# Performance work log

Hardware: AMD Instinct MI355X
Metric: run time of the kernel (lower is better)

## Reference

```python
import jax, jax.numpy as jnp
import numpy as np

NY, NX = 320, 320
NT = 160
SHOTS, NSRC, NREC = 2, 8, 96
DT = 4.0e-4
DH = 4.0
PML_W = 20
MAX_VEL = 1600.0
C1, C2 = 9.0 / 8.0, -1.0 / 24.0  # 4th-order staggered-grid FD coefficients


def _profile(n, w, d0):
    d = np.zeros(n, np.float64)
    i = np.arange(n, dtype=np.float64)
    d[:w] = d0 * ((w - i[:w]) / w) ** 2
    d[n - w:] = d0 * ((i[n - w:] - (n - 1 - w)) / w) ** 2
    return d


def _pml_b():
    # PML damping profile d(x) = d0*(x/L)^2, CPML decay factor b = exp(-d*dt)
    d0 = 3.0 * MAX_VEL * np.log(1000.0) / (2.0 * PML_W * DH)
    by = np.exp(-_profile(NY, PML_W, d0) * DT).astype(np.float32)
    bx = np.exp(-_profile(NX, PML_W, d0) * DT).astype(np.float32)
    return jnp.asarray(by)[None, :, None], jnp.asarray(bx)[None, None, :]


def _edge_mask():
    # mirrors zero_edges: kill wraparound contamination at the grid border
    m = np.ones((NY, NX), np.float32)
    m[:2, :] = 0.0
    m[-2:, :] = 0.0
    m[:, :2] = 0.0
    m[:, -2:] = 0.0
    return jnp.asarray(m)


def _d(f, axis, fwd):
    # staggered 4th-order forward (D+) / backward (D-) difference along axis
    if fwd:
        return (C1 * (jnp.roll(f, -1, axis) - f)
                + C2 * (jnp.roll(f, -2, axis) - jnp.roll(f, 1, axis))) * (1.0 / DH)
    return (C1 * (f - jnp.roll(f, 1, axis))
            + C2 * (jnp.roll(f, -1, axis) - jnp.roll(f, 2, axis))) * (1.0 / DH)


def _simulate(lamb, mu, buoyancy, amps, src_loc, rec_loc, checkpoint=False):
    by, bx = _pml_b()
    mask = _edge_mask()
    lam2mu = lamb + 2.0 * mu
    bidx = jnp.arange(SHOTS)[:, None]
    sy, sx = src_loc[..., 0], src_loc[..., 1]
    ry, rx = rec_loc[..., 0], rec_loc[..., 1]
    src_buoy = buoyancy[sy, sx]  # [shot, nsrc]
    zero = jnp.zeros((SHOTS, NY, NX), lamb.dtype)
    carry0 = tuple(zero for _ in range(13))

    def step(c, amp_t):
        (vy, vx, syy, sxy, sxx,
         mvyy, mvyx, mvxy, mvxx,
         msyyy, msxyy, msxyx, msxxx) = c
        # --- velocity update (with CPML memory variables) ---
        d = _d(syy, 1, False)
        msyyy = by * msyyy + (by - 1.0) * d
        ay = d + msyyy
        d = _d(sxy, 2, True)
        msxyx = bx * msxyx + (bx - 1.0) * d
        ay = ay + d + msxyx
        vy = vy + DT * buoyancy * ay
        d = _d(sxx, 2, False)
        msxxx = bx * msxxx + (bx - 1.0) * d
        ax = d + msxxx
        d = _d(sxy, 1, True)
        msxyy = by * msxyy + (by - 1.0) * d
        ax = ax + d + msxyy
        vx = vx + DT * buoyancy * ax
        # --- inject y-oriented sources into vy ---
        vy = vy.at[bidx, sy, sx].add(DT * amp_t * src_buoy)
        vy = vy * mask
        vx = vx * mask
        # --- stress update ---
        d = _d(vy, 1, True)
        mvyy = by * mvyy + (by - 1.0) * d
        e1 = d + mvyy
        d = _d(vx, 2, False)
        mvxx = bx * mvxx + (bx - 1.0) * d
        e2 = d + mvxx
        syy = (syy + DT * (lam2mu * e1 + lamb * e2)) * mask
        sxx = (sxx + DT * (lam2mu * e2 + lamb * e1)) * mask
        d = _d(vy, 2, True)
        mvyx = bx * mvyx + (bx - 1.0) * d
        g = d + mvyx
        d = _d(vx, 1, False)
        mvxy = by * mvxy + (by - 1.0) * d
        g = g + d + mvxy
        sxy = (sxy + DT * mu * g) * mask
        rec = vy[bidx, ry, rx]  # [shot, nrec]
        return (vy, vx, syy, sxy, sxx, mvyy, mvyx, mvxy, mvxx,
                msyyy, msxyy, msxyx, msxxx), rec

    f = jax.checkpoint(step) if checkpoint else step
    _, recs = jax.lax.scan(f, carry0, jnp.transpose(amps, (2, 0, 1)))
    # velocity receivers sampled at t+/-1/2 -> average adjacent time samples
    recs = (recs[1:] + recs[:-1]) * 0.5  # [nt-1, shot, nrec]
    return jnp.transpose(recs, (1, 2, 0))  # [shot, nrec, nt-1]


def setup_inputs() -> dict:
    key = jax.random.key(0)
    k1, k2, k3, k4, k5, k6 = jax.random.split(key, 6)
    u_l = jax.random.uniform(k1, (NY, NX), jnp.float32)
    u_m = jax.random.uniform(k2, (NY, NX), jnp.float32)
    u_b = jax.random.uniform(k3, (NY, NX), jnp.float32)
    lamb = (2.0e9 * (1.0 + 0.2 * u_l)).astype(jnp.float32)
    mu = (0.8e9 * (1.0 + 0.2 * u_m)).astype(jnp.float32)
    buoyancy = (1.0 / (1800.0 + 400.0 * u_b)).astype(jnp.float32)
    source_amplitudes_y = jax.random.normal(k4, (SHOTS, NSRC, NT), jnp.float32)
    source_locations_y = jax.random.randint(k5, (SHOTS, NSRC, 2), PML_W + 4, NY - PML_W - 4)
    receiver_locations_y = jax.random.randint(k6, (SHOTS, NREC, 2), PML_W + 4, NY - PML_W - 4)
    return {
        'lamb': lamb, 'mu': mu, 'buoyancy': buoyancy,
        'source_amplitudes_y': source_amplitudes_y,
        'source_locations_y': source_locations_y,
        'receiver_locations_y': receiver_locations_y,
    }


def reference(lamb, mu, buoyancy, source_amplitudes_y,
              source_locations_y, receiver_locations_y):
    return _simulate(lamb, mu, buoyancy, source_amplitudes_y,
                     source_locations_y, receiver_locations_y)
```

## Files before the change

kernel.cpp:

```cpp
#include <hip/hip_runtime.h>
#include <math.h>

constexpr int NY_ = 320, NX_ = 320, NT_ = 160, SHOTS_ = 2, NSRC_ = 8, NREC_ = 96;
constexpr float DT_  = 4.0e-4f;
constexpr float C1_  = 9.0f / 8.0f;
constexpr float C2_  = -1.0f / 24.0f;
constexpr float IDH_ = 0.25f;
constexpr int NP_     = NY_ * NX_;
constexpr int NSTRIP_ = 40;
constexpr int NBLK_   = SHOTS_ * NSTRIP_;
constexpr int REC_OFF_ = 8 * NP_;
constexpr int FLG_OFF_ = 8 * NP_ + SHOTS_ * NREC_ * NT_;
constexpr int WS_WORDS_ = FLG_OFF_ + 256;

__device__ __forceinline__ float cld(const float* p) {
    return __hip_atomic_load(p, __ATOMIC_RELAXED, __HIP_MEMORY_SCOPE_AGENT);
}
__device__ __forceinline__ void cst(float* p, float v) {
    __hip_atomic_store(p, v, __ATOMIC_RELAXED, __HIP_MEMORY_SCOPE_AGENT);
}
__device__ __forceinline__ unsigned cldu(const unsigned* p) {
    return __hip_atomic_load(p, __ATOMIC_RELAXED, __HIP_MEMORY_SCOPE_AGENT);
}
__device__ __forceinline__ void cstu(unsigned* p, unsigned v) {
    __hip_atomic_store(p, v, __ATOMIC_RELAXED, __HIP_MEMORY_SCOPE_AGENT);
}

__device__ __forceinline__ float gldf(const float* p, int y, int c) {
    return ((unsigned)y < (unsigned)NY_) ? cld(p + y * NX_ + c) : 0.0f;
}
__device__ __forceinline__ float ltap(const float (*A)[NX_], int ly, int c) {
    return ((unsigned)c < (unsigned)NX_) ? A[ly][c] : 0.0f;
}
__device__ __forceinline__ float shtap(float cur, float adj, int lane, int dx) {
    int idx = (lane + dx) & 63;
    float a = __shfl(cur, idx, 64);
    float b = __shfl(adj, idx, 64);
    return ((unsigned)(lane + dx) < 64u) ? a : b;
}

__device__ __forceinline__ void pollNbr(const unsigned* f, int sbase, int j,
                                        unsigned tgt, int tid) {
    __syncthreads();
    if (tid < 64) {
        for (;;) {
            bool ok = true;
            if (tid == 0 && j > 0)           ok = cldu(&f[sbase + j - 1]) >= tgt;
            else if (tid == 1 && j < NSTRIP_ - 1) ok = cldu(&f[sbase + j + 1]) >= tgt;
            if (__all(ok)) break;
            __builtin_amdgcn_s_sleep(1);
        }
    }
    __syncthreads();
    asm volatile("" ::: "memory");
}

__global__ void init_kernel(float* __restrict__ ws) {
    for (int i = blockIdx.x * 256 + threadIdx.x; i < WS_WORDS_; i += gridDim.x * 256)
        ws[i] = 0.0f;
}

__global__ __launch_bounds__(512)
void elastic_kernel(const float* __restrict__ lamb, const float* __restrict__ mu,
                    const float* __restrict__ buoy, const float* __restrict__ amps,
                    const int* __restrict__ src_loc, const int* __restrict__ rec_loc,
                    float* __restrict__ out, float* __restrict__ ws)
{
    __shared__ float Lvy[12][NX_], Lvx[12][NX_], Lsyy[12][NX_], Lsxy[12][NX_];

    const int tid  = threadIdx.x;
    const int lane = tid & 63;
    const int w    = tid >> 6;
    const int bid  = blockIdx.x;
    const int s    = bid / NSTRIP_;
    const int j    = bid % NSTRIP_;
    const int r0   = j * 8;
    const int gy   = r0 + w;
    const int ly   = w + 2;

    float* gVy  = ws + (0 * SHOTS_ + s) * NP_;
    float* gVx  = ws + (1 * SHOTS_ + s) * NP_;
    float* gSyy = ws + (2 * SHOTS_ + s) * NP_;
    float* gSxy = ws + (3 * SHOTS_ + s) * NP_;
    float* recp = ws + REC_OFF_ + (s * NREC_ + tid) * NT_;
    unsigned* flgV = (unsigned*)(ws + FLG_OFF_);
    unsigned* flgS = flgV + NBLK_;
    const int sbase = s * NSTRIP_;

    const double d0 = 3.0 * 1600.0 * log(1000.0) / (2.0 * 20.0 * 4.0);
    double py = 0.0;
    if (gy < 20)             { double u = (20.0 - gy) / 20.0;           py = u * u; }
    else if (gy >= NY_ - 20) { double u = (gy - (NY_ - 1 - 20)) / 20.0; py = u * u; }
    const float by = (float)exp(-d0 * py * 4.0e-4);
    const float bym1 = by - 1.0f;

    float bx[5], bxm1[5], mk[5], la[5], muv[5], bu[5], l2m[5];
    #pragma unroll
    for (int k = 0; k < 5; ++k) {
        int c = 64 * k + lane;
        double px = 0.0;
        if (c < 20)             { double u = (20.0 - c) / 20.0;           px = u * u; }
        else if (c >= NX_ - 20) { double u = (c - (NX_ - 1 - 20)) / 20.0; px = u * u; }
        bx[k] = (float)exp(-d0 * px * 4.0e-4);
        bxm1[k] = bx[k] - 1.0f;
        mk[k] = (gy < 2 || gy >= NY_ - 2 || c < 2 || c >= NX_ - 2) ? 0.0f : 1.0f;
        la[k]  = lamb[gy * NX_ + c];
        muv[k] = mu[gy * NX_ + c];
        bu[k]  = buoy[gy * NX_ + c];
        l2m[k] = la[k] + 2.0f * muv[k];
    }

    unsigned long long sm = 0ull;
    for (int js = 0; js < NSRC_; ++js) {
        int sy = src_loc[(s * NSRC_ + js) * 2 + 0];
        int sx = src_loc[(s * NSRC_ + js) * 2 + 1];
        if (sy == gy && (sx & 63) == lane) sm |= 1ull << (8 * (sx >> 6) + js);
    }
    bool myrec = false; int rl = 0;
    if (tid < NREC_) {
        int ry = rec_loc[(s * NREC_ + tid) * 2 + 0];
        int rx = rec_loc[(s * NREC_ + tid) * 2 + 1];
        if ((ry >> 3) == j) { myrec = true; rl = ((ry & 7) + 2) * NX_ + rx; }
    }

    for (int i = tid; i < 12 * NX_; i += 512) {
        ((float*)Lvy)[i] = 0.f; ((float*)Lvx)[i] = 0.f;
        ((float*)Lsyy)[i] = 0.f; ((float*)Lsxy)[i] = 0.f;
    }

    float vy[5] = {}, vx[5] = {}, syy[5] = {}, sxy[5] = {}, sxx[5] = {};
    float msyyy[5] = {}, msxyy[5] = {}, msxyx[5] = {}, msxxx[5] = {};
    float mvyy[5] = {}, mvyx[5] = {}, mvxy[5] = {}, mvxx[5] = {};

    for (int t = 0; t < NT_; ++t) {
        pollNbr(flgS, sbase, j, (unsigned)t, tid);

        if (tid < NX_) {
            int c = tid;
            float a0 = gldf(gSyy, r0 - 2, c), a1 = gldf(gSyy, r0 - 1, c), a2 = gldf(gSyy, r0 + 8, c);
            float b0 = gldf(gSxy, r0 - 1, c), b1 = gldf(gSxy, r0 + 8, c), b2 = gldf(gSxy, r0 + 9, c);
            Lsyy[0][c] = a0; Lsyy[1][c] = a1; Lsyy[10][c] = a2;
            Lsxy[1][c] = b0; Lsxy[10][c] = b1; Lsxy[11][c] = b2;
        }
        __syncthreads();

        #pragma unroll
        for (int k = 0; k < 5; ++k) {
            const int c = 64 * k + lane;
            const float sxxp = (k < 4) ? sxx[k + 1] : 0.0f;
            const float sxxm = (k > 0) ? sxx[k - 1] : 0.0f;
            float d, ay, ax;
            d = (C1_ * (syy[k] - Lsyy[ly - 1][c]) + C2_ * (Lsyy[ly + 1][c] - Lsyy[ly - 2][c])) * IDH_;
            msyyy[k] = by * msyyy[k] + bym1 * d;
            ay = d + msyyy[k];
            d = (C1_ * (ltap(Lsxy, ly, c + 1) - sxy[k])
               + C2_ * (ltap(Lsxy, ly, c + 2) - ltap(Lsxy, ly, c - 1))) * IDH_;
            msxyx[k] = bx[k] * msxyx[k] + bxm1[k] * d;
            ay = ay + d + msxyx[k];
            vy[k] = vy[k] + DT_ * bu[k] * ay;
            d = (C1_ * (sxx[k] - shtap(sxx[k], sxxm, lane, -1))
               + C2_ * (shtap(sxx[k], sxxp, lane, 1) - shtap(sxx[k], sxxm, lane, -2))) * IDH_;
            msxxx[k] = bx[k] * msxxx[k] + bxm1[k] * d;
            ax = d + msxxx[k];
            d = (C1_ * (Lsxy[ly + 1][c] - sxy[k]) + C2_ * (Lsxy[ly + 2][c] - Lsxy[ly - 1][c])) * IDH_;
            msxyy[k] = by * msxyy[k] + bym1 * d;
            ax = ax + d + msxyy[k];
            vx[k] = vx[k] + DT_ * bu[k] * ax;
            unsigned m = (unsigned)(sm >> (8 * k)) & 0xFFu;
            if (m) {
                for (int js = 0; js < NSRC_; ++js)
                    if (m & (1u << js)) vy[k] += DT_ * amps[(s * NSRC_ + js) * NT_ + t] * bu[k];
            }
            vy[k] *= mk[k]; vx[k] *= mk[k];
            Lvy[ly][c] = vy[k]; Lvx[ly][c] = vx[k];
        }
        __syncthreads();

        if (myrec) recp[t] = ((const float*)Lvy)[rl];

        if (tid < NX_) {
            int c = tid;
            float v0 = Lvy[2][c], v1 = Lvy[3][c], v2 = Lvy[9][c];
            float u0 = Lvx[2][c], u1 = Lvx[8][c], u2 = Lvx[9][c];
            cst(&gVy[(r0 + 0) * NX_ + c], v0);
            cst(&gVy[(r0 + 1) * NX_ + c], v1);
            cst(&gVy[(r0 + 7) * NX_ + c], v2);
            cst(&gVx[(r0 + 0) * NX_ + c], u0);
            cst(&gVx[(r0 + 6) * NX_ + c], u1);
            cst(&gVx[(r0 + 7) * NX_ + c], u2);
        }
        __syncthreads();
        if (tid == 0) {
            asm volatile("s_waitcnt vmcnt(0)" ::: "memory");
            cstu(&flgV[sbase + j], (unsigned)(t + 1));
        }

        pollNbr(flgV, sbase, j, (unsigned)(t + 1), tid);

        if (tid < NX_) {
            int c = tid;
            float a0 = gldf(gVy, r0 - 1, c), a1 = gldf(gVy, r0 + 8, c), a2 = gldf(gVy, r0 + 9, c);
            float b0 = gldf(gVx, r0 - 2, c), b1 = gldf(gVx, r0 - 1, c), b2 = gldf(gVx, r0 + 8, c);
            Lvy[1][c] = a0; Lvy[10][c] = a1; Lvy[11][c] = a2;
            Lvx[0][c] = b0; Lvx[1][c] = b1; Lvx[10][c] = b2;
        }
        __syncthreads();

        #pragma unroll
        for (int k = 0; k < 5; ++k) {
            const int c = 64 * k + lane;
            float d, e1, e2, g;
            d = (C1_ * (Lvy[ly + 1][c] - vy[k]) + C2_ * (Lvy[ly + 2][c] - Lvy[ly - 1][c])) * IDH_;
            mvyy[k] = by * mvyy[k] + bym1 * d;
            e1 = d + mvyy[k];
            d = (C1_ * (vx[k] - ltap(Lvx, ly, c - 1))
               + C2_ * (ltap(Lvx, ly, c + 1) - ltap(Lvx, ly, c - 2))) * IDH_;
            mvxx[k] = bx[k] * mvxx[k] + bxm1[k] * d;
            e2 = d + mvxx[k];
            syy[k] = (syy[k] + DT_ * (l2m[k] * e1 + la[k] * e2)) * mk[k];
            sxx[k] = (sxx[k] + DT_ * (l2m[k] * e2 + la[k] * e1)) * mk[k];
            d = (C1_ * (ltap(Lvy, ly, c + 1) - vy[k])
               + C2_ * (ltap(Lvy, ly, c + 2) - ltap(Lvy, ly, c - 1))) * IDH_;
            mvyx[k] = bx[k] * mvyx[k] + bxm1[k] * d;
            g = d + mvyx[k];
            d = (C1_ * (vx[k] - Lvx[ly - 1][c]) + C2_ * (Lvx[ly + 1][c] - Lvx[ly - 2][c])) * IDH_;
            mvxy[k] = by * mvxy[k] + bym1 * d;
            g = g + d + mvxy[k];
            sxy[k] = (sxy[k] + DT_ * muv[k] * g) * mk[k];
            Lsyy[ly][c] = syy[k]; Lsxy[ly][c] = sxy[k];
        }
        __syncthreads();

        if (tid < NX_) {
            int c = tid;
            float a0 = Lsyy[2][c], a1 = Lsyy[8][c], a2 = Lsyy[9][c];
            float b0 = Lsxy[2][c], b1 = Lsxy[3][c], b2 = Lsxy[9][c];
            cst(&gSyy[(r0 + 0) * NX_ + c], a0);
            cst(&gSyy[(r0 + 6) * NX_ + c], a1);
            cst(&gSyy[(r0 + 7) * NX_ + c], a2);
            cst(&gSxy[(r0 + 0) * NX_ + c], b0);
            cst(&gSxy[(r0 + 1) * NX_ + c], b1);
            cst(&gSxy[(r0 + 7) * NX_ + c], b2);
        }
        __syncthreads();
        if (tid == 0) {
            asm volatile("s_waitcnt vmcnt(0)" ::: "memory");
            cstu(&flgS[sbase + j], (unsigned)(t + 1));
        }
    }

    if (myrec) {
        float* op = out + (s * NREC_ + tid) * (NT_ - 1);
        for (int t = 0; t < NT_ - 1; ++t) op[t] = 0.5f * (recp[t] + recp[t + 1]);
    }
}

extern "C" void kernel_launch(void* const* d_in, const int* in_sizes, int n_in,
                              void* d_out, int out_size, void* d_ws, size_t ws_size,
                              hipStream_t stream)
{
    const float* lamb = (const float*)d_in[0];
    const float* mu   = (const float*)d_in[1];
    const float* buoy = (const float*)d_in[2];
    const float* amps = (const float*)d_in[3];
    const int*   src  = (const int*)d_in[4];
    const int*   recl = (const int*)d_in[5];
    float* out = (float*)d_out;
    float* ws  = (float*)d_ws;

    init_kernel<<<dim3(512), dim3(256), 0, stream>>>(ws);
    elastic_kernel<<<dim3(NBLK_), dim3(512), 0, stream>>>(lamb, mu, buoy, amps, src, recl, out, ws);
}
```

Before: 1.321 ms.

## Halve inter-block syncs per step via redundant halo-row velocity computation

Each block now runs 12 waves (768 threads) covering its 8 rows plus 2-row halos. It recomputes the velocity rows its neighbours own, so the per-timestep exchange shrinks to one stress-halo handoff instead of separate velocity and stress handoffs. Stress halo rows, including sxx, are written to double-buffered per-strip slots in the workspace rather than to full global fields. This cuts the neighbour flag polling and global round-trips per step from two to one, at the cost of redundant halo compute, larger blocks and more register/LDS pressure.

```diff
diff --git a/kernel.cpp b/kernel.cpp
--- a/kernel.cpp
+++ b/kernel.cpp
@@ -6,12 +6,16 @@
 constexpr float C1_  = 9.0f / 8.0f;
 constexpr float C2_  = -1.0f / 24.0f;
 constexpr float IDH_ = 0.25f;
-constexpr int NP_     = NY_ * NX_;
 constexpr int NSTRIP_ = 40;
 constexpr int NBLK_   = SHOTS_ * NSTRIP_;
-constexpr int REC_OFF_ = 8 * NP_;
-constexpr int FLG_OFF_ = 8 * NP_ + SHOTS_ * NREC_ * NT_;
+constexpr int HSLOT_   = 15 * NX_;
+constexpr int REC_OFF_ = 2 * SHOTS_ * NSTRIP_ * HSLOT_;
+constexpr int FLG_OFF_ = REC_OFF_ + SHOTS_ * NREC_ * NT_;
 constexpr int WS_WORDS_ = FLG_OFF_ + 256;
+
+__device__ __forceinline__ int hoff(int p, int s, int j) {
+    return ((p * SHOTS_ + s) * NSTRIP_ + j) * HSLOT_;
+}
 
 __device__ __forceinline__ float cld(const float* p) {
     return __hip_atomic_load(p, __ATOMIC_RELAXED, __HIP_MEMORY_SCOPE_AGENT);
@@ -26,9 +30,7 @@
     __hip_atomic_store(p, v, __ATOMIC_RELAXED, __HIP_MEMORY_SCOPE_AGENT);
 }
 
-__device__ __forceinline__ float gldf(const float* p, int y, int c) {
-    return ((unsigned)y < (unsigned)NY_) ? cld(p + y * NX_ + c) : 0.0f;
-}
+template <int R>
 __device__ __forceinline__ float ltap(const float (*A)[NX_], int ly, int c) {
     return ((unsigned)c < (unsigned)NX_) ? A[ly][c] : 0.0f;
 }
@@ -45,7 +47,7 @@
     if (tid < 64) {
         for (;;) {
             bool ok = true;
-            if (tid == 0 && j > 0)           ok = cldu(&f[sbase + j - 1]) >= tgt;
+            if (tid == 0 && j > 0)                ok = cldu(&f[sbase + j - 1]) >= tgt;
             else if (tid == 1 && j < NSTRIP_ - 1) ok = cldu(&f[sbase + j + 1]) >= tgt;
             if (__all(ok)) break;
             __builtin_amdgcn_s_sleep(1);
@@ -60,13 +62,13 @@
         ws[i] = 0.0f;
 }
 
-__global__ __launch_bounds__(512)
+__global__ __launch_bounds__(768)
 void elastic_kernel(const float* __restrict__ lamb, const float* __restrict__ mu,
                     const float* __restrict__ buoy, const float* __restrict__ amps,
                     const int* __restrict__ src_loc, const int* __restrict__ rec_loc,
                     float* __restrict__ out, float* __restrict__ ws)
 {
-    __shared__ float Lvy[12][NX_], Lvx[12][NX_], Lsyy[12][NX_], Lsxy[12][NX_];
+    __shared__ float Lsyy[14][NX_], Lsxy[14][NX_], Lvy[11][NX_], Lvx[11][NX_];
 
     const int tid  = threadIdx.x;
     const int lane = tid & 63;
@@ -75,16 +77,15 @@
     const int s    = bid / NSTRIP_;
     const int j    = bid % NSTRIP_;
     const int r0   = j * 8;
-    const int gy   = r0 + w;
-    const int ly   = w + 2;
-
-    float* gVy  = ws + (0 * SHOTS_ + s) * NP_;
-    float* gVx  = ws + (1 * SHOTS_ + s) * NP_;
-    float* gSyy = ws + (2 * SHOTS_ + s) * NP_;
-    float* gSxy = ws + (3 * SHOTS_ + s) * NP_;
+    const int gy   = r0 - 2 + w;
+    const int ys   = w + 1;
+    const bool doVy = (w >= 1);
+    const bool doVx = (w <= 10);
+    const bool doS  = (w >= 2 && w <= 9);
+
+    float* H = ws;
     float* recp = ws + REC_OFF_ + (s * NREC_ + tid) * NT_;
-    unsigned* flgV = (unsigned*)(ws + FLG_OFF_);
-    unsigned* flgS = flgV + NBLK_;
+    unsigned* flg = (unsigned*)(ws + FLG_OFF_);
     const int sbase = s * NSTRIP_;
 
     const double d0 = 3.0 * 1600.0 * log(1000.0) / (2.0 * 20.0 * 4.0);
@@ -93,6 +94,7 @@
     else if (gy >= NY_ - 20) { double u = (gy - (NY_ - 1 - 20)) / 20.0; py = u * u; }
     const float by = (float)exp(-d0 * py * 4.0e-4);
     const float bym1 = by - 1.0f;
+    const int gyc = gy < 0 ? 0 : (gy > NY_ - 1 ? NY_ - 1 : gy);
 
     float bx[5], bxm1[5], mk[5], la[5], muv[5], bu[5], l2m[5];
     #pragma unroll
@@ -104,9 +106,9 @@
         bx[k] = (float)exp(-d0 * px * 4.0e-4);
         bxm1[k] = bx[k] - 1.0f;
         mk[k] = (gy < 2 || gy >= NY_ - 2 || c < 2 || c >= NX_ - 2) ? 0.0f : 1.0f;
-        la[k]  = lamb[gy * NX_ + c];
-        muv[k] = mu[gy * NX_ + c];
-        bu[k]  = buoy[gy * NX_ + c];
+        la[k]  = lamb[gyc * NX_ + c];
+        muv[k] = mu[gyc * NX_ + c];
+        bu[k]  = buoy[gyc * NX_ + c];
         l2m[k] = la[k] + 2.0f * muv[k];
     }
 
@@ -116,136 +118,141 @@
         int sx = src_loc[(s * NSRC_ + js) * 2 + 1];
         if (sy == gy && (sx & 63) == lane) sm |= 1ull << (8 * (sx >> 6) + js);
     }
-    bool myrec = false; int rl = 0;
+    bool myrec = false; int rrow = 0, rx = 0;
     if (tid < NREC_) {
         int ry = rec_loc[(s * NREC_ + tid) * 2 + 0];
-        int rx = rec_loc[(s * NREC_ + tid) * 2 + 1];
-        if ((ry >> 3) == j) { myrec = true; rl = ((ry & 7) + 2) * NX_ + rx; }
-    }
-
-    for (int i = tid; i < 12 * NX_; i += 512) {
-        ((float*)Lvy)[i] = 0.f; ((float*)Lvx)[i] = 0.f;
-        ((float*)Lsyy)[i] = 0.f; ((float*)Lsxy)[i] = 0.f;
-    }
+        rx     = rec_loc[(s * NREC_ + tid) * 2 + 1];
+        if ((ry >> 3) == j) { myrec = true; rrow = ry - r0 + 1; }
+    }
+
+    for (int i = tid; i < 14 * NX_; i += 768) { ((float*)Lsyy)[i] = 0.f; ((float*)Lsxy)[i] = 0.f; }
+    for (int i = tid; i < 11 * NX_; i += 768) { ((float*)Lvy)[i] = 0.f; ((float*)Lvx)[i] = 0.f; }
 
     float vy[5] = {}, vx[5] = {}, syy[5] = {}, sxy[5] = {}, sxx[5] = {};
     float msyyy[5] = {}, msxyy[5] = {}, msxyx[5] = {}, msxxx[5] = {};
     float mvyy[5] = {}, mvyx[5] = {}, mvxy[5] = {}, mvxx[5] = {};
 
     for (int t = 0; t < NT_; ++t) {
-        pollNbr(flgS, sbase, j, (unsigned)t, tid);
+        pollNbr(flg, sbase, j, (unsigned)t, tid);
+        const int pi = (t + 1) & 1;
+        const int po = t & 1;
 
         if (tid < NX_) {
             int c = tid;
-            float a0 = gldf(gSyy, r0 - 2, c), a1 = gldf(gSyy, r0 - 1, c), a2 = gldf(gSyy, r0 + 8, c);
-            float b0 = gldf(gSxy, r0 - 1, c), b1 = gldf(gSxy, r0 + 8, c), b2 = gldf(gSxy, r0 + 9, c);
-            Lsyy[0][c] = a0; Lsyy[1][c] = a1; Lsyy[10][c] = a2;
-            Lsxy[1][c] = b0; Lsxy[10][c] = b1; Lsxy[11][c] = b2;
+            if (j > 0) {
+                const float* b = H + hoff(pi, s, j - 1);
+                float a0 = cld(b + 3 * NX_ + c), a1 = cld(b + 4 * NX_ + c), a2 = cld(b + 5 * NX_ + c);
+                float d0_ = cld(b + 9 * NX_ + c), d1 = cld(b + 10 * NX_ + c), d2 = cld(b + 11 * NX_ + c);
+                Lsyy[0][c] = a0; Lsyy[1][c] = a1; Lsyy[2][c] = a2;
+                Lsxy[0][c] = d0_; Lsxy[1][c] = d1; Lsxy[2][c] = d2;
+            }
+            if (j < NSTRIP_ - 1) {
+                const float* b = H + hoff(pi, s, j + 1);
+                float a0 = cld(b + 0 * NX_ + c), a1 = cld(b + 1 * NX_ + c), a2 = cld(b + 2 * NX_ + c);
+                float d0_ = cld(b + 6 * NX_ + c), d1 = cld(b + 7 * NX_ + c), d2 = cld(b + 8 * NX_ + c);
+                Lsyy[11][c] = a0; Lsyy[12][c] = a1; Lsyy[13][c] = a2;
+                Lsxy[11][c] = d0_; Lsxy[12][c] = d1; Lsxy[13][c] = d2;
+            }
+        }
+        if (w == 0 && j > 0) {
+            const float* b = H + hoff(pi, s, j - 1) + 13 * NX_;
+            #pragma unroll
+            for (int k = 0; k < 5; ++k) sxx[k] = cld(b + 64 * k + lane);
+        } else if (w == 1 && j > 0) {
+            const float* b = H + hoff(pi, s, j - 1) + 14 * NX_;
+            #pragma unroll
+            for (int k = 0; k < 5; ++k) sxx[k] = cld(b + 64 * k + lane);
+        } else if (w == 10 && j < NSTRIP_ - 1) {
+            const float* b = H + hoff(pi, s, j + 1) + 12 * NX_;
+            #pragma unroll
+            for (int k = 0; k < 5; ++k) sxx[k] = cld(b + 64 * k + lane);
         }
         __syncthreads();
 
-        #pragma unroll
-        for (int k = 0; k < 5; ++k) {
-            const int c = 64 * k + lane;
-            const float sxxp = (k < 4) ? sxx[k + 1] : 0.0f;
-            const float sxxm = (k > 0) ? sxx[k - 1] : 0.0f;
-            float d, ay, ax;
-            d = (C1_ * (syy[k] - Lsyy[ly - 1][c]) + C2_ * (Lsyy[ly + 1][c] - Lsyy[ly - 2][c])) * IDH_;
-            msyyy[k] = by * msyyy[k] + bym1 * d;
-            ay = d + msyyy[k];
-            d = (C1_ * (ltap(Lsxy, ly, c + 1) - sxy[k])
-               + C2_ * (ltap(Lsxy, ly, c + 2) - ltap(Lsxy, ly, c - 1))) * IDH_;
-            msxyx[k] = bx[k] * msxyx[k] + bxm1[k] * d;
-            ay = ay + d + msxyx[k];
-            vy[k] = vy[k] + DT_ * bu[k] * ay;
-            d = (C1_ * (sxx[k] - shtap(sxx[k], sxxm, lane, -1))
-               + C2_ * (shtap(sxx[k], sxxp, lane, 1) - shtap(sxx[k], sxxm, lane, -2))) * IDH_;
-            msxxx[k] = bx[k] * msxxx[k] + bxm1[k] * d;
-            ax = d + msxxx[k];
-            d = (C1_ * (Lsxy[ly + 1][c] - sxy[k]) + C2_ * (Lsxy[ly + 2][c] - Lsxy[ly - 1][c])) * IDH_;
-            msxyy[k] = by * msxyy[k] + bym1 * d;
-            ax = ax + d + msxyy[k];
-            vx[k] = vx[k] + DT_ * bu[k] * ax;
-            unsigned m = (unsigned)(sm >> (8 * k)) & 0xFFu;
-            if (m) {
-                for (int js = 0; js < NSRC_; ++js)
-                    if (m & (1u << js)) vy[k] += DT_ * amps[(s * NSRC_ + js) * NT_ + t] * bu[k];
-            }
-            vy[k] *= mk[k]; vx[k] *= mk[k];
-            Lvy[ly][c] = vy[k]; Lvx[ly][c] = vx[k];
+        if (doVy) {
+            #pragma unroll
+            for (int k = 0; k < 5; ++k) {
+                const int c = 64 * k + lane;
+                float d, ay;
+                d = (C1_ * (Lsyy[ys][c] - Lsyy[ys - 1][c]) + C2_ * (Lsyy[ys + 1][c] - Lsyy[ys - 2][c])) * IDH_;
+                msyyy[k] = by * msyyy[k] + bym1 * d;
+                ay = d + msyyy[k];
+                d = (C1_ * (ltap<0>(Lsxy, ys, c + 1) - Lsxy[ys][c])
+                   + C2_ * (ltap<0>(Lsxy, ys, c + 2) - ltap<0>(Lsxy, ys, c - 1))) * IDH_;
+                msxyx[k] = bx[k] * msxyx[k] + bxm1[k] * d;
+                ay = ay + d + msxyx[k];
+                vy[k] = vy[k] + DT_ * bu[k] * ay;
+                unsigned m = (unsigned)(sm >> (8 * k)) & 0xFFu;
+                if (m) {
+                    for (int js = 0; js < NSRC_; ++js)
+                        if (m & (1u << js)) vy[k] += DT_ * amps[(s * NSRC_ + js) * NT_ + t] * bu[k];
+                }
+                vy[k] *= mk[k];
+                Lvy[w - 1][c] = vy[k];
+            }
+        }
+        if (doVx) {
+            #pragma unroll
+            for (int k = 0; k < 5; ++k) {
+                const int c = 64 * k + lane;
+                const float sxxp = (k < 4) ? sxx[k + 1] : 0.0f;
+                const float sxxm = (k > 0) ? sxx[k - 1] : 0.0f;
+                float d, ax;
+                d = (C1_ * (sxx[k] - shtap(sxx[k], sxxm, lane, -1))
+                   + C2_ * (shtap(sxx[k], sxxp, lane, 1) - shtap(sxx[k], sxxm, lane, -2))) * IDH_;
+                msxxx[k] = bx[k] * msxxx[k] + bxm1[k] * d;
+                ax = d + msxxx[k];
+                d = (C1_ * (Lsxy[ys + 1][c] - Lsxy[ys][c]) + C2_ * (Lsxy[ys + 2][c] - Lsxy[ys - 1][c])) * IDH_;
+                msxyy[k] = by * msxyy[k] + bym1 * d;
+                ax = ax + d + msxyy[k];
+                vx[k] = vx[k] + DT_ * bu[k] * ax;
+                vx[k] *= mk[k];
+                Lvx[w][c] = vx[k];
+            }
         }
         __syncthreads();
 
-        if (myrec) recp[t] = ((const float*)Lvy)[rl];
-
-        if (tid < NX_) {
-            int c = tid;
-            float v0 = Lvy[2][c], v1 = Lvy[3][c], v2 = Lvy[9][c];
-            float u0 = Lvx[2][c], u1 = Lvx[8][c], u2 = Lvx[9][c];
-            cst(&gVy[(r0 + 0) * NX_ + c], v0);
-            cst(&gVy[(r0 + 1) * NX_ + c], v1);
-            cst(&gVy[(r0 + 7) * NX_ + c], v2);
-            cst(&gVx[(r0 + 0) * NX_ + c], u0);
-            cst(&gVx[(r0 + 6) * NX_ + c], u1);
-            cst(&gVx[(r0 + 7) * NX_ + c], u2);
+        if (myrec) recp[t] = Lvy[rrow][rx];
+
+        if (doS) {
+            const int yv = w - 1, xv = w;
+            float* Hj = H + hoff(po, s, j);
+            const int slotS = (w <= 4) ? (w - 2) : (w - 4);
+            #pragma unroll
+            for (int k = 0; k < 5; ++k) {
+                const int c = 64 * k + lane;
+                float d, e1, e2, g;
+                d = (C1_ * (Lvy[yv + 1][c] - vy[k]) + C2_ * (Lvy[yv + 2][c] - Lvy[yv - 1][c])) * IDH_;
+                mvyy[k] = by * mvyy[k] + bym1 * d;
+                e1 = d + mvyy[k];
+                d = (C1_ * (vx[k] - ltap<0>(Lvx, xv, c - 1))
+                   + C2_ * (ltap<0>(Lvx, xv, c + 1) - ltap<0>(Lvx, xv, c - 2))) * IDH_;
+                mvxx[k] = bx[k] * mvxx[k] + bxm1[k] * d;
+                e2 = d + mvxx[k];
+                syy[k] = (syy[k] + DT_ * (l2m[k] * e1 + la[k] * e2)) * mk[k];
+                sxx[k] = (sxx[k] + DT_ * (l2m[k] * e2 + la[k] * e1)) * mk[k];
+                d = (C1_ * (ltap<0>(Lvy, yv, c + 1) - vy[k])
+                   + C2_ * (ltap<0>(Lvy, yv, c + 2) - ltap<0>(Lvy, yv, c - 1))) * IDH_;
+                mvyx[k] = bx[k] * mvyx[k] + bxm1[k] * d;
+                g = d + mvyx[k];
+                d = (C1_ * (vx[k] - Lvx[xv - 1][c]) + C2_ * (Lvx[xv + 1][c] - Lvx[xv - 2][c])) * IDH_;
+                mvxy[k] = by * mvxy[k] + bym1 * d;
+                g = g + d + mvxy[k];
+                sxy[k] = (sxy[k] + DT_ * muv[k] * g) * mk[k];
+                Lsyy[ys][c] = syy[k]; Lsxy[ys][c] = sxy[k];
+                if (w <= 4 || w >= 7) {
+                    cst(Hj + slotS * NX_ + c, syy[k]);
+                    cst(Hj + (6 + slotS) * NX_ + c, sxy[k]);
+                }
+                if (w == 2) cst(Hj + 12 * NX_ + c, sxx[k]);
+                else if (w == 8) cst(Hj + 13 * NX_ + c, sxx[k]);
+                else if (w == 9) cst(Hj + 14 * NX_ + c, sxx[k]);
+            }
         }
         __syncthreads();
         if (tid == 0) {
             asm volatile("s_waitcnt vmcnt(0)" ::: "memory");
-            cstu(&flgV[sbase + j], (unsigned)(t + 1));
-        }
-
-        pollNbr(flgV, sbase, j, (unsigned)(t + 1), tid);
-
-        if (tid < NX_) {
-            int c = tid;
-            float a0 = gldf(gVy, r0 - 1, c), a1 = gldf(gVy, r0 + 8, c), a2 = gldf(gVy, r0 + 9, c);
-            float b0 = gldf(gVx, r0 - 2, c), b1 = gldf(gVx, r0 - 1, c), b2 = gldf(gVx, r0 + 8, c);
-            Lvy[1][c] = a0; Lvy[10][c] = a1; Lvy[11][c] = a2;
-            Lvx[0][c] = b0; Lvx[1][c] = b1; Lvx[10][c] = b2;
-        }
-        __syncthreads();
-
-        #pragma unroll
-        for (int k = 0; k < 5; ++k) {
-            const int c = 64 * k + lane;
-            float d, e1, e2, g;
-            d = (C1_ * (Lvy[ly + 1][c] - vy[k]) + C2_ * (Lvy[ly + 2][c] - Lvy[ly - 1][c])) * IDH_;
-            mvyy[k] = by * mvyy[k] + bym1 * d;
-            e1 = d + mvyy[k];
-            d = (C1_ * (vx[k] - ltap(Lvx, ly, c - 1))
-               + C2_ * (ltap(Lvx, ly, c + 1) - ltap(Lvx, ly, c - 2))) * IDH_;
-            mvxx[k] = bx[k] * mvxx[k] + bxm1[k] * d;
-            e2 = d + mvxx[k];
-            syy[k] = (syy[k] + DT_ * (l2m[k] * e1 + la[k] * e2)) * mk[k];
-            sxx[k] = (sxx[k] + DT_ * (l2m[k] * e2 + la[k] * e1)) * mk[k];
-            d = (C1_ * (ltap(Lvy, ly, c + 1) - vy[k])
-               + C2_ * (ltap(Lvy, ly, c + 2) - ltap(Lvy, ly, c - 1))) * IDH_;
-            mvyx[k] = bx[k] * mvyx[k] + bxm1[k] * d;
-            g = d + mvyx[k];
-            d = (C1_ * (vx[k] - Lvx[ly - 1][c]) + C2_ * (Lvx[ly + 1][c] - Lvx[ly - 2][c])) * IDH_;
-            mvxy[k] = by * mvxy[k] + bym1 * d;
-            g = g + d + mvxy[k];
-            sxy[k] = (sxy[k] + DT_ * muv[k] * g) * mk[k];
-            Lsyy[ly][c] = syy[k]; Lsxy[ly][c] = sxy[k];
-        }
-        __syncthreads();
-
-        if (tid < NX_) {
-            int c = tid;
-            float a0 = Lsyy[2][c], a1 = Lsyy[8][c], a2 = Lsyy[9][c];
-            float b0 = Lsxy[2][c], b1 = Lsxy[3][c], b2 = Lsxy[9][c];
-            cst(&gSyy[(r0 + 0) * NX_ + c], a0);
-            cst(&gSyy[(r0 + 6) * NX_ + c], a1);
-            cst(&gSyy[(r0 + 7) * NX_ + c], a2);
-            cst(&gSxy[(r0 + 0) * NX_ + c], b0);
-            cst(&gSxy[(r0 + 1) * NX_ + c], b1);
-            cst(&gSxy[(r0 + 7) * NX_ + c], b2);
-        }
-        __syncthreads();
-        if (tid == 0) {
-            asm volatile("s_waitcnt vmcnt(0)" ::: "memory");
-            cstu(&flgS[sbase + j], (unsigned)(t + 1));
+            cstu(&flg[sbase + j], (unsigned)(t + 1));
         }
     }
 
@@ -269,5 +276,5 @@
     float* ws  = (float*)d_ws;
 
     init_kernel<<<dim3(512), dim3(256), 0, stream>>>(ws);
-    elastic_kernel<<<dim3(NBLK_), dim3(512), 0, stream>>>(lamb, mu, buoy, amps, src, recl, out, ws);
-}
+    elastic_kernel<<<dim3(NBLK_), dim3(768), 0, stream>>>(lamb, mu, buoy, amps, src, recl, out, ws);
+}
```

After: 1.935 ms. +46.5%, slower.

## Replace block barriers with per-wave LDS flags and double-buffered halo slots

Applied to the files above, without the earlier changes.

Removes all __syncthreads from the time loop. Waves now coordinate through per-wave LDS flags with acquire/release, and only the boundary waves (0,1,6,7) exchange halos with neighbouring strips. That exchange goes through compact double-buffered slot buffers with per-role global flags instead of full-grid arrays. x-direction stencil taps now use wavefront shuffles of register values instead of LDS reads, and receivers are recorded directly from registers. The goal is to cut block-wide barrier and polling latency so interior waves can run ahead, at the cost of more complex fine-grained spin-waiting and a higher risk of memory-ordering bugs.

```diff
diff --git a/kernel.cpp b/kernel.cpp
--- a/kernel.cpp
+++ b/kernel.cpp
@@ -6,12 +6,14 @@
 constexpr float C1_  = 9.0f / 8.0f;
 constexpr float C2_  = -1.0f / 24.0f;
 constexpr float IDH_ = 0.25f;
-constexpr int NP_     = NY_ * NX_;
 constexpr int NSTRIP_ = 40;
 constexpr int NBLK_   = SHOTS_ * NSTRIP_;
-constexpr int REC_OFF_ = 8 * NP_;
-constexpr int FLG_OFF_ = 8 * NP_ + SHOTS_ * NREC_ * NT_;
-constexpr int WS_WORDS_ = FLG_OFF_ + 256;
+constexpr int SLOT_    = 6 * NX_;
+constexpr int VS_OFF_  = 0;
+constexpr int SS_OFF_  = VS_OFF_ + 2 * SHOTS_ * NSTRIP_ * SLOT_;
+constexpr int REC_OFF_ = SS_OFF_ + 2 * SHOTS_ * NSTRIP_ * SLOT_;
+constexpr int GF_OFF_  = REC_OFF_ + SHOTS_ * NREC_ * NT_;
+constexpr int WS_WORDS_ = GF_OFF_ + 8 * NBLK_ + 64;
 
 __device__ __forceinline__ float cld(const float* p) {
     return __hip_atomic_load(p, __ATOMIC_RELAXED, __HIP_MEMORY_SCOPE_AGENT);
@@ -25,12 +27,15 @@
 __device__ __forceinline__ void cstu(unsigned* p, unsigned v) {
     __hip_atomic_store(p, v, __ATOMIC_RELAXED, __HIP_MEMORY_SCOPE_AGENT);
 }
-
-__device__ __forceinline__ float gldf(const float* p, int y, int c) {
-    return ((unsigned)y < (unsigned)NY_) ? cld(p + y * NX_ + c) : 0.0f;
-}
-__device__ __forceinline__ float ltap(const float (*A)[NX_], int ly, int c) {
-    return ((unsigned)c < (unsigned)NX_) ? A[ly][c] : 0.0f;
+__device__ __forceinline__ void lwait(const unsigned* f, unsigned tgt) {
+    while (__hip_atomic_load(f, __ATOMIC_ACQUIRE, __HIP_MEMORY_SCOPE_WORKGROUP) < tgt) {}
+}
+__device__ __forceinline__ void lpost(unsigned* f, unsigned v) {
+    __hip_atomic_store(f, v, __ATOMIC_RELEASE, __HIP_MEMORY_SCOPE_WORKGROUP);
+}
+__device__ __forceinline__ void gwait2(const unsigned* a, const unsigned* b, unsigned tgt) {
+    while (cldu(a) < tgt || cldu(b) < tgt) __builtin_amdgcn_s_sleep(1);
+    asm volatile("" ::: "memory");
 }
 __device__ __forceinline__ float shtap(float cur, float adj, int lane, int dx) {
     int idx = (lane + dx) & 63;
@@ -39,53 +44,26 @@
     return ((unsigned)(lane + dx) < 64u) ? a : b;
 }
 
-__device__ __forceinline__ void pollNbr(const unsigned* f, int sbase, int j,
-                                        unsigned tgt, int tid) {
-    __syncthreads();
-    if (tid < 64) {
-        for (;;) {
-            bool ok = true;
-            if (tid == 0 && j > 0)           ok = cldu(&f[sbase + j - 1]) >= tgt;
-            else if (tid == 1 && j < NSTRIP_ - 1) ok = cldu(&f[sbase + j + 1]) >= tgt;
-            if (__all(ok)) break;
-            __builtin_amdgcn_s_sleep(1);
-        }
-    }
-    __syncthreads();
-    asm volatile("" ::: "memory");
-}
-
 __global__ void init_kernel(float* __restrict__ ws) {
     for (int i = blockIdx.x * 256 + threadIdx.x; i < WS_WORDS_; i += gridDim.x * 256)
         ws[i] = 0.0f;
 }
 
-__global__ __launch_bounds__(512)
+__global__ __launch_bounds__(512, 2)
 void elastic_kernel(const float* __restrict__ lamb, const float* __restrict__ mu,
                     const float* __restrict__ buoy, const float* __restrict__ amps,
                     const int* __restrict__ src_loc, const int* __restrict__ rec_loc,
                     float* __restrict__ out, float* __restrict__ ws)
 {
-    __shared__ float Lvy[12][NX_], Lvx[12][NX_], Lsyy[12][NX_], Lsxy[12][NX_];
-
-    const int tid  = threadIdx.x;
-    const int lane = tid & 63;
-    const int w    = tid >> 6;
-    const int bid  = blockIdx.x;
-    const int s    = bid / NSTRIP_;
-    const int j    = bid % NSTRIP_;
-    const int r0   = j * 8;
-    const int gy   = r0 + w;
-    const int ly   = w + 2;
-
-    float* gVy  = ws + (0 * SHOTS_ + s) * NP_;
-    float* gVx  = ws + (1 * SHOTS_ + s) * NP_;
-    float* gSyy = ws + (2 * SHOTS_ + s) * NP_;
-    float* gSxy = ws + (3 * SHOTS_ + s) * NP_;
-    float* recp = ws + REC_OFF_ + (s * NREC_ + tid) * NT_;
-    unsigned* flgV = (unsigned*)(ws + FLG_OFF_);
-    unsigned* flgS = flgV + NBLK_;
-    const int sbase = s * NSTRIP_;
+    __shared__ float Lsyy[12][NX_], Lsxy[12][NX_], Lvy[12][NX_], Lvx[12][NX_];
+    __shared__ unsigned vF[8], sF[8], hF[4];
+
+    const int tid = threadIdx.x, lane = tid & 63, w = tid >> 6;
+    const int bid = blockIdx.x, s = bid / NSTRIP_, j = bid % NSTRIP_;
+    const int r0 = j * 8, gy = r0 + w, yi = w + 2;
+    const int sj = s * NSTRIP_ + j;
+    unsigned* gV = (unsigned*)(ws + GF_OFF_);
+    unsigned* gS = gV + 4 * NBLK_;
 
     const double d0 = 3.0 * 1600.0 * log(1000.0) / (2.0 * 20.0 * 4.0);
     double py = 0.0;
@@ -109,60 +87,91 @@
         bu[k]  = buoy[gy * NX_ + c];
         l2m[k] = la[k] + 2.0f * muv[k];
     }
-
     unsigned long long sm = 0ull;
     for (int js = 0; js < NSRC_; ++js) {
         int sy = src_loc[(s * NSRC_ + js) * 2 + 0];
         int sx = src_loc[(s * NSRC_ + js) * 2 + 1];
         if (sy == gy && (sx & 63) == lane) sm |= 1ull << (8 * (sx >> 6) + js);
     }
-    bool myrec = false; int rl = 0;
-    if (tid < NREC_) {
-        int ry = rec_loc[(s * NREC_ + tid) * 2 + 0];
-        int rx = rec_loc[(s * NREC_ + tid) * 2 + 1];
-        if ((ry >> 3) == j) { myrec = true; rl = ((ry & 7) + 2) * NX_ + rx; }
-    }
+    int nrec = 0, recid[8], reck[8];
+    for (int r = 0; r < NREC_; ++r) {
+        int ry = rec_loc[(s * NREC_ + r) * 2 + 0];
+        int rx = rec_loc[(s * NREC_ + r) * 2 + 1];
+        if (ry == gy && (rx & 63) == lane && nrec < 8) { recid[nrec] = r; reck[nrec] = rx >> 6; ++nrec; }
+    }
+    float* recbase = ws + REC_OFF_;
 
     for (int i = tid; i < 12 * NX_; i += 512) {
-        ((float*)Lvy)[i] = 0.f; ((float*)Lvx)[i] = 0.f;
         ((float*)Lsyy)[i] = 0.f; ((float*)Lsxy)[i] = 0.f;
-    }
+        ((float*)Lvy)[i]  = 0.f; ((float*)Lvx)[i]  = 0.f;
+    }
+    if (tid < 8) { vF[tid] = 0u; sF[tid] = 0u; }
+    if (tid < 4) hF[tid] = 0u;
+    __syncthreads();
 
     float vy[5] = {}, vx[5] = {}, syy[5] = {}, sxy[5] = {}, sxx[5] = {};
     float msyyy[5] = {}, msxyy[5] = {}, msxyx[5] = {}, msxxx[5] = {};
     float mvyy[5] = {}, mvyx[5] = {}, mvxy[5] = {}, mvxx[5] = {};
 
     for (int t = 0; t < NT_; ++t) {
-        pollNbr(flgS, sbase, j, (unsigned)t, tid);
-
-        if (tid < NX_) {
-            int c = tid;
-            float a0 = gldf(gSyy, r0 - 2, c), a1 = gldf(gSyy, r0 - 1, c), a2 = gldf(gSyy, r0 + 8, c);
-            float b0 = gldf(gSxy, r0 - 1, c), b1 = gldf(gSxy, r0 + 8, c), b2 = gldf(gSxy, r0 + 9, c);
-            Lsyy[0][c] = a0; Lsyy[1][c] = a1; Lsyy[10][c] = a2;
-            Lsxy[1][c] = b0; Lsxy[10][c] = b1; Lsxy[11][c] = b2;
-        }
-        __syncthreads();
+        const unsigned ut = (unsigned)t;
+        const int pi = (t + 1) & 1, po = t & 1;
+
+        if (w == 0) {
+            if (j > 0) {
+                lwait(&vF[1], ut);
+                gwait2(&gS[2 * NBLK_ + (sj - 1)], &gS[3 * NBLK_ + (sj - 1)], ut);
+                const float* B = ws + SS_OFF_ + ((pi * SHOTS_ + s) * NSTRIP_ + (j - 1)) * SLOT_;
+                #pragma unroll
+                for (int k = 0; k < 5; ++k) {
+                    int c = 64 * k + lane;
+                    float a = cld(B + 3 * NX_ + c), b = cld(B + 4 * NX_ + c), e = cld(B + 5 * NX_ + c);
+                    Lsyy[0][c] = a; Lsyy[1][c] = b; Lsxy[1][c] = e;
+                }
+            }
+            lpost(&hF[0], ut + 1u);
+        } else if (w == 7) {
+            if (j < NSTRIP_ - 1) {
+                lwait(&vF[6], ut);
+                gwait2(&gS[0 * NBLK_ + (sj + 1)], &gS[1 * NBLK_ + (sj + 1)], ut);
+                const float* B = ws + SS_OFF_ + ((pi * SHOTS_ + s) * NSTRIP_ + (j + 1)) * SLOT_;
+                #pragma unroll
+                for (int k = 0; k < 5; ++k) {
+                    int c = 64 * k + lane;
+                    float a = cld(B + 0 * NX_ + c), b = cld(B + 1 * NX_ + c), e = cld(B + 2 * NX_ + c);
+                    Lsyy[10][c] = a; Lsxy[10][c] = b; Lsxy[11][c] = e;
+                }
+            }
+            lpost(&hF[1], ut + 1u);
+        }
+        if (w == 1) lwait(&hF[0], ut + 1u);
+        if (w == 6) lwait(&hF[1], ut + 1u);
+        if (w >= 2) lwait(&sF[w - 2], ut);
+        if (w >= 1) lwait(&sF[w - 1], ut);
+        if (w <= 6) lwait(&sF[w + 1], ut);
+        if (w <= 5) lwait(&sF[w + 2], ut);
 
         #pragma unroll
         for (int k = 0; k < 5; ++k) {
             const int c = 64 * k + lane;
-            const float sxxp = (k < 4) ? sxx[k + 1] : 0.0f;
-            const float sxxm = (k > 0) ? sxx[k - 1] : 0.0f;
+            const float sxyP = (k < 4) ? sxy[k + 1] : 0.0f;
+            const float sxyM = (k > 0) ? sxy[k - 1] : 0.0f;
+            const float sxxP = (k < 4) ? sxx[k + 1] : 0.0f;
+            const float sxxM = (k > 0) ? sxx[k - 1] : 0.0f;
             float d, ay, ax;
-            d = (C1_ * (syy[k] - Lsyy[ly - 1][c]) + C2_ * (Lsyy[ly + 1][c] - Lsyy[ly - 2][c])) * IDH_;
+            d = (C1_ * (syy[k] - Lsyy[yi - 1][c]) + C2_ * (Lsyy[yi + 1][c] - Lsyy[yi - 2][c])) * IDH_;
             msyyy[k] = by * msyyy[k] + bym1 * d;
             ay = d + msyyy[k];
-            d = (C1_ * (ltap(Lsxy, ly, c + 1) - sxy[k])
-               + C2_ * (ltap(Lsxy, ly, c + 2) - ltap(Lsxy, ly, c - 1))) * IDH_;
+            d = (C1_ * (shtap(sxy[k], sxyP, lane, 1) - sxy[k])
+               + C2_ * (shtap(sxy[k], sxyP, lane, 2) - shtap(sxy[k], sxyM, lane, -1))) * IDH_;
             msxyx[k] = bx[k] * msxyx[k] + bxm1[k] * d;
             ay = ay + d + msxyx[k];
             vy[k] = vy[k] + DT_ * bu[k] * ay;
-            d = (C1_ * (sxx[k] - shtap(sxx[k], sxxm, lane, -1))
-               + C2_ * (shtap(sxx[k], sxxp, lane, 1) - shtap(sxx[k], sxxm, lane, -2))) * IDH_;
+            d = (C1_ * (sxx[k] - shtap(sxx[k], sxxM, lane, -1))
+               + C2_ * (shtap(sxx[k], sxxP, lane, 1) - shtap(sxx[k], sxxM, lane, -2))) * IDH_;
             msxxx[k] = bx[k] * msxxx[k] + bxm1[k] * d;
             ax = d + msxxx[k];
-            d = (C1_ * (Lsxy[ly + 1][c] - sxy[k]) + C2_ * (Lsxy[ly + 2][c] - Lsxy[ly - 1][c])) * IDH_;
+            d = (C1_ * (Lsxy[yi + 1][c] - sxy[k]) + C2_ * (Lsxy[yi + 2][c] - Lsxy[yi - 1][c])) * IDH_;
             msxyy[k] = by * msxyy[k] + bym1 * d;
             ax = ax + d + msxyy[k];
             vx[k] = vx[k] + DT_ * bu[k] * ax;
@@ -172,86 +181,110 @@
                     if (m & (1u << js)) vy[k] += DT_ * amps[(s * NSRC_ + js) * NT_ + t] * bu[k];
             }
             vy[k] *= mk[k]; vx[k] *= mk[k];
-            Lvy[ly][c] = vy[k]; Lvx[ly][c] = vx[k];
-        }
-        __syncthreads();
-
-        if (myrec) recp[t] = ((const float*)Lvy)[rl];
-
-        if (tid < NX_) {
-            int c = tid;
-            float v0 = Lvy[2][c], v1 = Lvy[3][c], v2 = Lvy[9][c];
-            float u0 = Lvx[2][c], u1 = Lvx[8][c], u2 = Lvx[9][c];
-            cst(&gVy[(r0 + 0) * NX_ + c], v0);
-            cst(&gVy[(r0 + 1) * NX_ + c], v1);
-            cst(&gVy[(r0 + 7) * NX_ + c], v2);
-            cst(&gVx[(r0 + 0) * NX_ + c], u0);
-            cst(&gVx[(r0 + 6) * NX_ + c], u1);
-            cst(&gVx[(r0 + 7) * NX_ + c], u2);
-        }
-        __syncthreads();
-        if (tid == 0) {
+            Lvy[yi][c] = vy[k]; Lvx[yi][c] = vx[k];
+        }
+        lpost(&vF[w], ut + 1u);
+        for (int i = 0; i < nrec; ++i)
+            recbase[(s * NREC_ + recid[i]) * NT_ + t] = vy[reck[i]];
+
+        if (w == 0 || w == 1 || w == 6 || w == 7) {
+            float* P = ws + VS_OFF_ + ((po * SHOTS_ + s) * NSTRIP_ + j) * SLOT_;
+            #pragma unroll
+            for (int k = 0; k < 5; ++k) {
+                int c = 64 * k + lane;
+                if (w == 0) { cst(P + 0 * NX_ + c, vy[k]); cst(P + 1 * NX_ + c, vx[k]); }
+                else if (w == 1) cst(P + 2 * NX_ + c, vy[k]);
+                else if (w == 6) cst(P + 3 * NX_ + c, vx[k]);
+                else { cst(P + 4 * NX_ + c, vy[k]); cst(P + 5 * NX_ + c, vx[k]); }
+            }
             asm volatile("s_waitcnt vmcnt(0)" ::: "memory");
-            cstu(&flgV[sbase + j], (unsigned)(t + 1));
-        }
-
-        pollNbr(flgV, sbase, j, (unsigned)(t + 1), tid);
-
-        if (tid < NX_) {
-            int c = tid;
-            float a0 = gldf(gVy, r0 - 1, c), a1 = gldf(gVy, r0 + 8, c), a2 = gldf(gVy, r0 + 9, c);
-            float b0 = gldf(gVx, r0 - 2, c), b1 = gldf(gVx, r0 - 1, c), b2 = gldf(gVx, r0 + 8, c);
-            Lvy[1][c] = a0; Lvy[10][c] = a1; Lvy[11][c] = a2;
-            Lvx[0][c] = b0; Lvx[1][c] = b1; Lvx[10][c] = b2;
-        }
-        __syncthreads();
+            const int role = (w == 0) ? 0 : (w == 1) ? 1 : (w == 6) ? 2 : 3;
+            cstu(&gV[role * NBLK_ + sj], ut + 1u);
+        }
+
+        if (w == 0) {
+            if (j > 0) {
+                lwait(&sF[1], ut);
+                gwait2(&gV[2 * NBLK_ + (sj - 1)], &gV[3 * NBLK_ + (sj - 1)], ut + 1u);
+                const float* B = ws + VS_OFF_ + ((po * SHOTS_ + s) * NSTRIP_ + (j - 1)) * SLOT_;
+                #pragma unroll
+                for (int k = 0; k < 5; ++k) {
+                    int c = 64 * k + lane;
+                    float a = cld(B + 3 * NX_ + c), b = cld(B + 4 * NX_ + c), e = cld(B + 5 * NX_ + c);
+                    Lvx[0][c] = a; Lvy[1][c] = b; Lvx[1][c] = e;
+                }
+            }
+            lpost(&hF[2], ut + 1u);
+        } else if (w == 7) {
+            if (j < NSTRIP_ - 1) {
+                lwait(&sF[6], ut);
+                gwait2(&gV[0 * NBLK_ + (sj + 1)], &gV[1 * NBLK_ + (sj + 1)], ut + 1u);
+                const float* B = ws + VS_OFF_ + ((po * SHOTS_ + s) * NSTRIP_ + (j + 1)) * SLOT_;
+                #pragma unroll
+                for (int k = 0; k < 5; ++k) {
+                    int c = 64 * k + lane;
+                    float a = cld(B + 0 * NX_ + c), b = cld(B + 1 * NX_ + c), e = cld(B + 2 * NX_ + c);
+                    Lvy[10][c] = a; Lvx[10][c] = b; Lvy[11][c] = e;
+                }
+            }
+            lpost(&hF[3], ut + 1u);
+        }
+        if (w == 1) lwait(&hF[2], ut + 1u);
+        if (w == 6) lwait(&hF[3], ut + 1u);
+        if (w >= 2) lwait(&vF[w - 2], ut + 1u);
+        if (w >= 1) lwait(&vF[w - 1], ut + 1u);
+        if (w <= 6) lwait(&vF[w + 1], ut + 1u);
+        if (w <= 5) lwait(&vF[w + 2], ut + 1u);
 
         #pragma unroll
         for (int k = 0; k < 5; ++k) {
             const int c = 64 * k + lane;
+            const float vyP = (k < 4) ? vy[k + 1] : 0.0f;
+            const float vyM = (k > 0) ? vy[k - 1] : 0.0f;
+            const float vxP = (k < 4) ? vx[k + 1] : 0.0f;
+            const float vxM = (k > 0) ? vx[k - 1] : 0.0f;
             float d, e1, e2, g;
-            d = (C1_ * (Lvy[ly + 1][c] - vy[k]) + C2_ * (Lvy[ly + 2][c] - Lvy[ly - 1][c])) * IDH_;
+            d = (C1_ * (Lvy[yi + 1][c] - vy[k]) + C2_ * (Lvy[yi + 2][c] - Lvy[yi - 1][c])) * IDH_;
             mvyy[k] = by * mvyy[k] + bym1 * d;
             e1 = d + mvyy[k];
-            d = (C1_ * (vx[k] - ltap(Lvx, ly, c - 1))
-               + C2_ * (ltap(Lvx, ly, c + 1) - ltap(Lvx, ly, c - 2))) * IDH_;
+            d = (C1_ * (vx[k] - shtap(vx[k], vxM, lane, -1))
+               + C2_ * (shtap(vx[k], vxP, lane, 1) - shtap(vx[k], vxM, lane, -2))) * IDH_;
             mvxx[k] = bx[k] * mvxx[k] + bxm1[k] * d;
             e2 = d + mvxx[k];
             syy[k] = (syy[k] + DT_ * (l2m[k] * e1 + la[k] * e2)) * mk[k];
             sxx[k] = (sxx[k] + DT_ * (l2m[k] * e2 + la[k] * e1)) * mk[k];
-            d = (C1_ * (ltap(Lvy, ly, c + 1) - vy[k])
-               + C2_ * (ltap(Lvy, ly, c + 2) - ltap(Lvy, ly, c - 1))) * IDH_;
+            d = (C1_ * (shtap(vy[k], vyP, lane, 1) - vy[k])
+               + C2_ * (shtap(vy[k], vyP, lane, 2) - shtap(vy[k], vyM, lane, -1))) * IDH_;
             mvyx[k] = bx[k] * mvyx[k] + bxm1[k] * d;
             g = d + mvyx[k];
-            d = (C1_ * (vx[k] - Lvx[ly - 1][c]) + C2_ * (Lvx[ly + 1][c] - Lvx[ly - 2][c])) * IDH_;
+            d = (C1_ * (vx[k] - Lvx[yi - 1][c]) + C2_ * (Lvx[yi + 1][c] - Lvx[yi - 2][c])) * IDH_;
             mvxy[k] = by * mvxy[k] + bym1 * d;
             g = g + d + mvxy[k];
             sxy[k] = (sxy[k] + DT_ * muv[k] * g) * mk[k];
-            Lsyy[ly][c] = syy[k]; Lsxy[ly][c] = sxy[k];
-        }
-        __syncthreads();
-
-        if (tid < NX_) {
-            int c = tid;
-            float a0 = Lsyy[2][c], a1 = Lsyy[8][c], a2 = Lsyy[9][c];
-            float b0 = Lsxy[2][c], b1 = Lsxy[3][c], b2 = Lsxy[9][c];
-            cst(&gSyy[(r0 + 0) * NX_ + c], a0);
-            cst(&gSyy[(r0 + 6) * NX_ + c], a1);
-            cst(&gSyy[(r0 + 7) * NX_ + c], a2);
-            cst(&gSxy[(r0 + 0) * NX_ + c], b0);
-            cst(&gSxy[(r0 + 1) * NX_ + c], b1);
-            cst(&gSxy[(r0 + 7) * NX_ + c], b2);
-        }
-        __syncthreads();
-        if (tid == 0) {
+            Lsyy[yi][c] = syy[k]; Lsxy[yi][c] = sxy[k];
+        }
+        lpost(&sF[w], ut + 1u);
+
+        if (w == 0 || w == 1 || w == 6 || w == 7) {
+            float* P = ws + SS_OFF_ + ((po * SHOTS_ + s) * NSTRIP_ + j) * SLOT_;
+            #pragma unroll
+            for (int k = 0; k < 5; ++k) {
+                int c = 64 * k + lane;
+                if (w == 0) { cst(P + 0 * NX_ + c, syy[k]); cst(P + 1 * NX_ + c, sxy[k]); }
+                else if (w == 1) cst(P + 2 * NX_ + c, sxy[k]);
+                else if (w == 6) cst(P + 3 * NX_ + c, syy[k]);
+                else { cst(P + 4 * NX_ + c, syy[k]); cst(P + 5 * NX_ + c, sxy[k]); }
+            }
             asm volatile("s_waitcnt vmcnt(0)" ::: "memory");
-            cstu(&flgS[sbase + j], (unsigned)(t + 1));
-        }
-    }
-
-    if (myrec) {
-        float* op = out + (s * NREC_ + tid) * (NT_ - 1);
-        for (int t = 0; t < NT_ - 1; ++t) op[t] = 0.5f * (recp[t] + recp[t + 1]);
+            const int role = (w == 0) ? 0 : (w == 1) ? 1 : (w == 6) ? 2 : 3;
+            cstu(&gS[role * NBLK_ + sj], ut + 1u);
+        }
+    }
+
+    for (int i = 0; i < nrec; ++i) {
+        const float* rp = recbase + (s * NREC_ + recid[i]) * NT_;
+        float* op = out + (s * NREC_ + recid[i]) * (NT_ - 1);
+        for (int t = 0; t < NT_ - 1; ++t) op[t] = 0.5f * (rp[t] + rp[t + 1]);
     }
 }
 
```

Result: slower. 1.475 ms (+11.7%).
